# Optimization experiments

Measured on AMD Instinct MI355X. Metric: run time of the kernel, lower is better.

The kernel has to match this reference:

```python
import jax, jax.numpy as jnp
import numpy as np
from jax import lax

B, L, D, H = 48, 512, 384, 384


def setup_inputs() -> dict:
    key = jax.random.key(0)
    ks = jax.random.split(key, 8)
    def w(k, shape, fan):
        return jax.random.normal(k, shape, jnp.float32) / np.float32(np.sqrt(fan))
    return {
        "v": jax.random.normal(ks[0], (B, L, D), jnp.float32),
        "mask": jnp.ones((B, L), jnp.bool_),
        "Wp_cur": w(ks[1], (D, H), D),      # torch Wp (applied to v_i)
        "Wp_seq": w(ks[2], (D, H), D),      # torch Wp_ (applied to all of v)
        "V": w(ks[3], (H,), H),             # torch V: Linear(H, 1, bias=False)
        "W_ih": w(ks[4], (3 * H, 2 * D), 2 * D),  # GRUCell input weights
        "W_hh": w(ks[5], (3 * H, H), H),           # GRUCell hidden weights
        "b_ih": jnp.zeros((3 * H,), jnp.float32),
        "b_hh": jnp.zeros((3 * H,), jnp.float32),
    }


def _forward(v, mask, Wp_cur, Wp_seq, V, W_ih, W_hh, b_ih, b_hh):
    Bv, Lv, _ = v.shape
    Hh = W_hh.shape[1]
    # Torch recomputes Wp_(v) identically every step; hoist it (same math).
    Wpv = jnp.einsum('bld,dh->blh', v, Wp_seq)            # [B,L,H]
    neg = jnp.where(mask, 0.0, -1e30).astype(v.dtype)     # additive attention mask [B,L]

    def step(h, vi):                                       # vi: [B,D], h: [B,H]
        wpi = vi @ Wp_cur                                  # [B,H]
        x = jnp.tanh(Wpv + wpi[:, None, :])                # [B,L,H]
        s = jnp.einsum('blh,h->bl', x, V) + neg            # scores [B,L]
        a = jax.nn.softmax(s, axis=1)                      # masked softmax
        c = jnp.einsum('bl,bld->bd', a, v)                 # context [B,D]
        r = jnp.concatenate([vi, c], axis=1)               # [B,2D]
        gi = r @ W_ih.T + b_ih
        gh = h @ W_hh.T + b_hh
        ir, iz, inn = jnp.split(gi, 3, axis=1)
        hr, hz, hn = jnp.split(gh, 3, axis=1)
        rg = jax.nn.sigmoid(ir + hr)
        zg = jax.nn.sigmoid(iz + hz)
        ng = jnp.tanh(inn + rg * hn)
        hnew = (1.0 - zg) * ng + zg * h                    # PyTorch GRUCell update
        return hnew, hnew

    h0 = jnp.zeros((Bv, Hh), v.dtype)
    h_last, hs = lax.scan(jax.checkpoint(step), h0, jnp.swapaxes(v, 0, 1))
    hs = jnp.swapaxes(hs, 0, 1)                            # [B,L,H]
    # dropout p=0.0 -> identity; h = hs[:, -1]
    return hs, h_last


def reference(v, mask, Wp_cur, Wp_seq, V, W_ih, W_hh, b_ih, b_hh):
    return _forward(v, mask, Wp_cur, Wp_seq, V, W_ih, W_hh, b_ih, b_hh)
```

## Files before the change

### kernel.cpp

```cpp
#include <hip/hip_runtime.h>


typedef unsigned short u16;
typedef unsigned int u32;
typedef short short8 __attribute__((ext_vector_type(8)));
typedef float f32x4 __attribute__((ext_vector_type(4)));
typedef float f4 __attribute__((ext_vector_type(4)));
typedef _Float16 h2_t __attribute__((ext_vector_type(2)));
typedef _Float16 h8_t __attribute__((ext_vector_type(8)));

#define BDIM 48
#define LDIM 512
#define DDIM 384
#define HDIM 384

__device__ __forceinline__ float bf2f(u16 u) { return __uint_as_float(((u32)u) << 16); }
__device__ __forceinline__ u16 f2bf(float f) {
  u32 x = __float_as_uint(f);
  u32 r = (x + 0x7fffu + ((x >> 16) & 1u)) >> 16;
  return (u16)r;
}
__device__ __forceinline__ float sigm(float x) {
  return __builtin_amdgcn_rcpf(1.f + exp2f(-1.4426950408889634f * x));
}
__device__ __forceinline__ float tanh_f(float x) {
  float e = exp2f(2.885390081777927f * x);
  return 1.f - 2.f * __builtin_amdgcn_rcpf(e + 1.f);
}

__device__ __forceinline__ void load16(const void* src, long ld, int isf32,
                                       long row, int kbase, short8& o0, short8& o1)
{
  if (isf32) {
    const float* s = (const float*)src + row * ld + kbase;
    f4 q0 = *(const f4*)(s);
    f4 q1 = *(const f4*)(s + 4);
    f4 q2 = *(const f4*)(s + 8);
    f4 q3 = *(const f4*)(s + 12);
    short8 a, b;
    a[0] = (short)f2bf(q0[0]); a[1] = (short)f2bf(q0[1]);
    a[2] = (short)f2bf(q0[2]); a[3] = (short)f2bf(q0[3]);
    a[4] = (short)f2bf(q1[0]); a[5] = (short)f2bf(q1[1]);
    a[6] = (short)f2bf(q1[2]); a[7] = (short)f2bf(q1[3]);
    b[0] = (short)f2bf(q2[0]); b[1] = (short)f2bf(q2[1]);
    b[2] = (short)f2bf(q2[2]); b[3] = (short)f2bf(q2[3]);
    b[4] = (short)f2bf(q3[0]); b[5] = (short)f2bf(q3[1]);
    b[6] = (short)f2bf(q3[2]); b[7] = (short)f2bf(q3[3]);
    o0 = a; o1 = b;
  } else {
    const u16* s = (const u16*)src + row * ld + kbase;
    o0 = *(const short8*)s;
    o1 = *(const short8*)(s + 8);
  }
}

__global__ __launch_bounds__(256) void gemm_bt(
    const void* __restrict__ A1, const void* __restrict__ A2,
    long lda1, long lda2, int ksplit, int a1f, int a2f,
    const void* __restrict__ Bm, long ldb, int bfm,
    u16* __restrict__ Out, int N, int K,
    long strideA, long strideB, long strideO,
    const float* __restrict__ bias, int epi_exp2, int out_bf16)
{
  __shared__ u16 As[128][40];
  __shared__ u16 Bs[128][40];
  const int tid = threadIdx.x;
  const int lane = tid & 63;
  const int w = tid >> 6;
  const int wm = w >> 1, wn = w & 1;
  const int l15 = lane & 15, quad = lane >> 4;
  const long m0 = (long)blockIdx.x * 128;
  const long n0 = (long)blockIdx.y * 128;
  const int z = blockIdx.z;
  const char* A1p = (const char*)A1 + (long)z * strideA * (a1f ? 4 : 2);
  const char* A2p = (const char*)A2 + (long)z * strideA * (a2f ? 4 : 2);
  const char* Bp  = (const char*)Bm + (long)z * strideB * (bfm ? 4 : 2);
  u16* Op = Out + (long)z * strideO;

  const int r2 = tid & 127;
  const int half = tid >> 7;

  f32x4 acc[4][4];
#pragma unroll
  for (int a = 0; a < 4; a++)
#pragma unroll
    for (int c = 0; c < 4; c++) acc[a][c] = (f32x4){0.f, 0.f, 0.f, 0.f};

  for (int k0 = 0; k0 < K; k0 += 32) {
    const void* srcA; long lda; int kk; int af;
    if (k0 < ksplit) { srcA = A1p; lda = lda1; kk = k0; af = a1f; }
    else             { srcA = A2p; lda = lda2; kk = k0 - ksplit; af = a2f; }
    short8 a0, a1, b0, b1;
    load16(srcA, lda, af, m0 + r2, kk + half * 16, a0, a1);
    load16(Bp, ldb, bfm, n0 + r2, k0 + half * 16, b0, b1);
    __syncthreads();
    *(short8*)&As[r2][half * 16] = a0;
    *(short8*)&As[r2][half * 16 + 8] = a1;
    *(short8*)&Bs[r2][half * 16] = b0;
    *(short8*)&Bs[r2][half * 16 + 8] = b1;
    __syncthreads();
    short8 af_[4], bf_[4];
#pragma unroll
    for (int mt = 0; mt < 4; mt++) af_[mt] = *(const short8*)&As[wm * 64 + mt * 16 + l15][quad * 8];
#pragma unroll
    for (int nt = 0; nt < 4; nt++) bf_[nt] = *(const short8*)&Bs[wn * 64 + nt * 16 + l15][quad * 8];
#pragma unroll
    for (int mt = 0; mt < 4; mt++)
#pragma unroll
      for (int nt = 0; nt < 4; nt++)
        acc[mt][nt] = __builtin_amdgcn_mfma_f32_16x16x32_bf16(af_[mt], bf_[nt], acc[mt][nt], 0, 0, 0);
  }

#pragma unroll
  for (int mt = 0; mt < 4; mt++) {
#pragma unroll
    for (int nt = 0; nt < 4; nt++) {
      const long col = n0 + wn * 64 + nt * 16 + l15;
      float bv = bias ? bias[col] : 0.f;
#pragma unroll
      for (int rg = 0; rg < 4; rg++) {
        long row = m0 + wm * 64 + mt * 16 + quad * 4 + rg;
        float vv = acc[mt][nt][rg] + bv;
        if (epi_exp2) {
          float t = vv * 2.885390081777927f;
          t = fminf(fmaxf(t, -15.9f), 15.9f);
          vv = exp2f(t);
        }
        long idx = row * (long)N + col;
        if (out_bf16) Op[idx] = f2bf(vv);
        else ((_Float16*)Op)[idx] = (_Float16)vv;
      }
    }
  }
}

__global__ void transpose_f2b(const float* __restrict__ src, u16* __restrict__ dst,
                              int rows, int cols, long sstride, long dstride)
{
  __shared__ float t[32][33];
  const int bz = blockIdx.z;
  const float* s = src + (long)bz * sstride;
  u16* d = dst + (long)bz * dstride;
  const int c0 = blockIdx.x * 32, r0 = blockIdx.y * 32;
  const int tx = threadIdx.x, ty = threadIdx.y;
#pragma unroll
  for (int j = 0; j < 4; j++) t[ty + j * 8][tx] = s[(long)(r0 + ty + j * 8) * cols + c0 + tx];
  __syncthreads();
#pragma unroll
  for (int j = 0; j < 4; j++) d[(long)(c0 + ty + j * 8) * rows + r0 + tx] = f2bf(t[tx][ty + j * 8]);
}

__global__ __launch_bounds__(256) void attn_softmax(
    const _Float16* __restrict__ E, const _Float16* __restrict__ F,
    const float* __restrict__ Vw, u16* __restrict__ Aout)
{
  const int blk = blockIdx.x;
  const int x8 = blk & 7;
  const int rest = blk >> 3;
  const int i = rest & 511;
  const int b = x8 + 8 * (rest >> 9);
  const int tid = threadIdx.x;
  const int lane = tid & 63, w = tid >> 6;
  const int r = lane & 15, sub = lane >> 4;
  __shared__ float Tl[512];
  __shared__ float red[8];

  const h8_t* Fr = (const h8_t*)(F + ((long)b * LDIM + i) * HDIM + r * 24);
  h8_t fq0 = Fr[0], fq1 = Fr[1], fq2 = Fr[2];
  float fv[24], vv[24];
#pragma unroll
  for (int j = 0; j < 8; j++) {
    fv[j] = (float)fq0[j]; fv[8 + j] = (float)fq1[j]; fv[16 + j] = (float)fq2[j];
  }
  const float* Vp = Vw + r * 24;
#pragma unroll
  for (int j = 0; j < 24; j++) vv[j] = Vp[j];

  for (int li = 0; li < 32; ++li) {
    const int l = li * 16 + w * 4 + sub;
    const h8_t* Er = (const h8_t*)(E + ((long)b * LDIM + l) * HDIM + r * 24);
    h8_t e0 = Er[0], e1 = Er[1], e2 = Er[2];
    float p = 0.f;
#pragma unroll
    for (int j = 0; j < 8; j++) {
      p += vv[j]      * __builtin_amdgcn_rcpf((float)e0[j] * fv[j]      + 1.f);
      p += vv[8 + j]  * __builtin_amdgcn_rcpf((float)e1[j] * fv[8 + j]  + 1.f);
      p += vv[16 + j] * __builtin_amdgcn_rcpf((float)e2[j] * fv[16 + j] + 1.f);
    }
    p += __shfl_xor(p, 1);
    p += __shfl_xor(p, 2);
    p += __shfl_xor(p, 4);
    p += __shfl_xor(p, 8);
    if (r == 0) Tl[l] = p;
  }
  __syncthreads();

  const float t0 = Tl[tid], t1 = Tl[tid + 256];
  float mn = fminf(t0, t1);
#pragma unroll
  for (int off = 32; off; off >>= 1) mn = fminf(mn, __shfl_xor(mn, off));
  if (lane == 0) red[w] = mn;
  __syncthreads();
  const float mT = fminf(fminf(red[0], red[1]), fminf(red[2], red[3]));
  const float C2 = 2.885390081777927f;
  float p0 = exp2f(C2 * (mT - t0));
  float p1 = exp2f(C2 * (mT - t1));
  float ssum = p0 + p1;
#pragma unroll
  for (int off = 32; off; off >>= 1) ssum += __shfl_xor(ssum, off);
  if (lane == 0) red[4 + w] = ssum;
  __syncthreads();
  const float Z = (red[4] + red[5]) + (red[6] + red[7]);
  const float inv = __builtin_amdgcn_rcpf(Z);
  u16* Ar = Aout + ((long)b * LDIM + i) * LDIM;
  Ar[tid] = f2bf(p0 * inv);
  Ar[tid + 256] = f2bf(p1 * inv);
}

__global__ __launch_bounds__(512, 2) void recurrence(
    const float* __restrict__ Whh, const float* __restrict__ bhh_g,
    const _Float16* __restrict__ GI, u32* __restrict__ hslots,
    float* __restrict__ out)
{
  const int blk = blockIdx.x;
  const int x8 = blk & 7;
  const int s = blk >> 3;
  const int b = x8 + 8 * (s % 6);
  const int g = s / 6;
  const int tid = threadIdx.x;
  const int tx = tid & 15;
  const int ty = tid >> 4;

  __shared__ _Float16 hall[HDIM];
  __shared__ float gh[288];

  h2_t wv[9][12];
  float bh[9];
#pragma unroll
  for (int q = 0; q < 9; q++) {
    int rr = ty * 9 + q;
    int R = (rr / 96) * 384 + g * 96 + (rr % 96);
    const f4* wq = (const f4*)(Whh + (long)R * HDIM + tx * 24);
#pragma unroll
    for (int t6 = 0; t6 < 6; t6++) {
      f4 u = wq[t6];
      wv[q][2 * t6]     = (h2_t){(_Float16)u[0], (_Float16)u[1]};
      wv[q][2 * t6 + 1] = (h2_t){(_Float16)u[2], (_Float16)u[3]};
    }
    bh[q] = (tx == 0) ? bhh_g[R] : 0.f;
  }

  if (tid < HDIM) hall[tid] = (_Float16)0.f;
  __syncthreads();

  const long gi_base = (long)b * LDIM * 1152;
  const int own = tid >> 5;
  (void)own;
  float hprev = 0.f;

  for (int i = 0; i < LDIM; ++i) {
    float gir = 0.f, giz = 0.f, gin = 0.f;
    if (tid < 96) {
      const long gb = gi_base + (long)i * 1152 + g * 96 + tid;
      gir = (float)GI[gb];
      giz = (float)GI[gb + 384];
      gin = (float)GI[gb + 768];
    }

    if (i > 0) {
      if (tid < HDIM && (tid / 96) != g) {
        u32* p = hslots + (long)(i & 1) * (BDIM * HDIM) + (long)b * HDIM + tid;
        u32 val = __hip_atomic_load(p, __ATOMIC_RELAXED, __HIP_MEMORY_SCOPE_AGENT);
        while ((val >> 16) != (u32)i) {
          __builtin_amdgcn_s_sleep(1);
          val = __hip_atomic_load(p, __ATOMIC_RELAXED, __HIP_MEMORY_SCOPE_AGENT);
        }
        union { u16 u; _Float16 h; } cv;
        cv.u = (u16)val;
        hall[tid] = cv.h;
      }
      __syncthreads();
    }

    h2_t hv[12];
#pragma unroll
    for (int p = 0; p < 12; p++) hv[p] = *(const h2_t*)&hall[tx * 24 + 2 * p];
    float ac[9];
#pragma unroll
    for (int q = 0; q < 9; q++) {
      float a = 0.f;
#pragma unroll
      for (int p = 0; p < 12; p++) a = __builtin_amdgcn_fdot2(wv[q][p], hv[p], a, false);
      ac[q] = a;
    }
#pragma unroll
    for (int q = 0; q < 9; q++) {
      float a = ac[q];
      a += __shfl_xor(a, 1);
      a += __shfl_xor(a, 2);
      a += __shfl_xor(a, 4);
      a += __shfl_xor(a, 8);
      if (tx == 0) gh[ty * 9 + q] = a + bh[q];
    }
    __syncthreads();
    if (tid < 96) {
      const int j = g * 96 + tid;
      float hr = gh[tid], hz = gh[96 + tid], hn = gh[192 + tid];
      float rg = sigm(gir + hr);
      float zg = sigm(giz + hz);
      float ng = tanh_f(gin + rg * hn);
      float hnew = (1.f - zg) * ng + zg * hprev;
      hprev = hnew;
      out[((long)b * LDIM + i) * HDIM + j] = hnew;
      if (i == LDIM - 1) out[(long)BDIM * LDIM * HDIM + (long)b * HDIM + j] = hnew;
      union { _Float16 h; u16 u; } cv;
      cv.h = (_Float16)hnew;
      hall[j] = cv.h;
      if (i + 1 < LDIM) {
        u32 val = ((u32)(i + 1) << 16) | (u32)cv.u;
        __hip_atomic_store(
            hslots + (long)((i + 1) & 1) * (BDIM * HDIM) + (long)b * HDIM + j, val,
            __ATOMIC_RELAXED, __HIP_MEMORY_SCOPE_AGENT);
      }
    }
  }
}

extern "C" void kernel_launch(void* const* d_in, const int* in_sizes, int n_in,
                              void* d_out, int out_size, void* d_ws, size_t ws_size,
                              hipStream_t stream)
{
  (void)in_sizes; (void)n_in; (void)out_size; (void)ws_size;
  const float* v      = (const float*)d_in[0];
  const float* Wp_cur = (const float*)d_in[2];
  const float* Wp_seq = (const float*)d_in[3];
  const float* Vw     = (const float*)d_in[4];
  const float* W_ih   = (const float*)d_in[5];
  const float* W_hh   = (const float*)d_in[6];
  const float* b_ih   = (const float*)d_in[7];
  const float* b_hh   = (const float*)d_in[8];
  float* out = (float*)d_out;

  char* ws = (char*)d_ws;
  size_t off = 0;
  auto alloc = [&](size_t bytes) -> char* {
    char* p = ws + off;
    off += (bytes + 255) & ~(size_t)255;
    return p;
  };
  u32* hslots = (u32*)alloc((size_t)2 * 48 * 384 * 4);
  u16* WpSeqT = (u16*)alloc((size_t)384 * 384 * 2);
  u16* WpCurT = (u16*)alloc((size_t)384 * 384 * 2);
  u16* Cbuf   = (u16*)alloc((size_t)24576 * 384 * 2);
  u16* vT     = (u16*)alloc((size_t)48 * 384 * 512 * 2);
  char* region = alloc((size_t)24576 * 384 * 2 * 2 + (size_t)24576 * 512 * 2);
  _Float16* E  = (_Float16*)region;
  _Float16* F  = (_Float16*)(region + (size_t)24576 * 384 * 2);
  u16* Abuf    = (u16*)(region + (size_t)24576 * 384 * 2 * 2);
  _Float16* GI = (_Float16*)region;

  transpose_f2b<<<dim3(12, 12, 1), dim3(32, 8), 0, stream>>>(Wp_seq, WpSeqT, 384, 384, 0, 0);
  transpose_f2b<<<dim3(12, 12, 1), dim3(32, 8), 0, stream>>>(Wp_cur, WpCurT, 384, 384, 0, 0);
  transpose_f2b<<<dim3(12, 16, 48), dim3(32, 8), 0, stream>>>(v, vT, 512, 384,
                                                              (long)512 * 384, (long)384 * 512);

  gemm_bt<<<dim3(192, 3, 1), 256, 0, stream>>>(v, v, 384, 384, 1 << 30, 1, 1,
                                               WpSeqT, 384, 0,
                                               (u16*)E, 384, 384, 0, 0, 0, nullptr, 1, 0);
  gemm_bt<<<dim3(192, 3, 1), 256, 0, stream>>>(v, v, 384, 384, 1 << 30, 1, 1,
                                               WpCurT, 384, 0,
                                               (u16*)F, 384, 384, 0, 0, 0, nullptr, 1, 0);

  attn_softmax<<<dim3(24576), 256, 0, stream>>>(E, F, Vw, Abuf);

  gemm_bt<<<dim3(4, 3, 48), 256, 0, stream>>>(Abuf, Abuf, 512, 512, 1 << 30, 0, 0,
                                              vT, 512, 0,
                                              Cbuf, 384, 512,
                                              (long)512 * 512, (long)384 * 512, (long)512 * 384,
                                              nullptr, 0, 1);

  gemm_bt<<<dim3(192, 9, 1), 256, 0, stream>>>(v, Cbuf, 384, 384, 384, 1, 0,
                                               W_ih, 768, 1,
                                               (u16*)GI, 1152, 768, 0, 0, 0, b_ih, 0, 0);

  void* args[] = {(void*)&W_hh, (void*)&b_hh, (void*)&GI, (void*)&hslots, (void*)&out};
  hipLaunchCooperativeKernel(recurrence, dim3(192), dim3(512), args, 0, stream);
}
```

Baseline: 2.342 ms.

## Tile four query rows per attention block and prefetch GI in recurrence

```diff
diff --git a/kernel.cpp b/kernel.cpp
--- a/kernel.cpp
+++ b/kernel.cpp
@@ -19,6 +19,9 @@
   u32 x = __float_as_uint(f);
   u32 r = (x + 0x7fffu + ((x >> 16) & 1u)) >> 16;
   return (u16)r;
+}
+__device__ __forceinline__ float h16f(u16 u) {
+  union { u16 u; _Float16 h; } c; c.u = u; return (float)c.h;
 }
 __device__ __forceinline__ float sigm(float x) {
   return __builtin_amdgcn_rcpf(1.f + exp2f(-1.4426950408889634f * x));
@@ -157,20 +160,23 @@
   const int blk = blockIdx.x;
   const int x8 = blk & 7;
   const int rest = blk >> 3;
-  const int i = rest & 511;
-  const int b = x8 + 8 * (rest >> 9);
+  const int ig = rest & 127;
+  const int b = x8 + 8 * (rest >> 7);
+  const int i0 = ig * 4;
   const int tid = threadIdx.x;
   const int lane = tid & 63, w = tid >> 6;
   const int r = lane & 15, sub = lane >> 4;
-  __shared__ float Tl[512];
-  __shared__ float red[8];
-
-  const h8_t* Fr = (const h8_t*)(F + ((long)b * LDIM + i) * HDIM + r * 24);
-  h8_t fq0 = Fr[0], fq1 = Fr[1], fq2 = Fr[2];
-  float fv[24], vv[24];
-#pragma unroll
-  for (int j = 0; j < 8; j++) {
-    fv[j] = (float)fq0[j]; fv[8 + j] = (float)fq1[j]; fv[16 + j] = (float)fq2[j];
+  __shared__ float Tl[4][512];
+
+  float fv[4][24], vv[24];
+#pragma unroll
+  for (int ii = 0; ii < 4; ii++) {
+    const h8_t* Fr = (const h8_t*)(F + ((long)b * LDIM + i0 + ii) * HDIM + r * 24);
+    h8_t q0 = Fr[0], q1 = Fr[1], q2 = Fr[2];
+#pragma unroll
+    for (int j = 0; j < 8; j++) {
+      fv[ii][j] = (float)q0[j]; fv[ii][8 + j] = (float)q1[j]; fv[ii][16 + j] = (float)q2[j];
+    }
   }
   const float* Vp = Vw + r * 24;
 #pragma unroll
@@ -180,46 +186,51 @@
     const int l = li * 16 + w * 4 + sub;
     const h8_t* Er = (const h8_t*)(E + ((long)b * LDIM + l) * HDIM + r * 24);
     h8_t e0 = Er[0], e1 = Er[1], e2 = Er[2];
-    float p = 0.f;
+    float ev[24];
 #pragma unroll
     for (int j = 0; j < 8; j++) {
-      p += vv[j]      * __builtin_amdgcn_rcpf((float)e0[j] * fv[j]      + 1.f);
-      p += vv[8 + j]  * __builtin_amdgcn_rcpf((float)e1[j] * fv[8 + j]  + 1.f);
-      p += vv[16 + j] * __builtin_amdgcn_rcpf((float)e2[j] * fv[16 + j] + 1.f);
-    }
-    p += __shfl_xor(p, 1);
-    p += __shfl_xor(p, 2);
-    p += __shfl_xor(p, 4);
-    p += __shfl_xor(p, 8);
-    if (r == 0) Tl[l] = p;
+      ev[j] = (float)e0[j]; ev[8 + j] = (float)e1[j]; ev[16 + j] = (float)e2[j];
+    }
+    float p[4] = {0.f, 0.f, 0.f, 0.f};
+#pragma unroll
+    for (int j = 0; j < 24; j++) {
+#pragma unroll
+      for (int ii = 0; ii < 4; ii++)
+        p[ii] += vv[j] * __builtin_amdgcn_rcpf(ev[j] * fv[ii][j] + 1.f);
+    }
+#pragma unroll
+    for (int ii = 0; ii < 4; ii++) {
+      float q = p[ii];
+      q += __shfl_xor(q, 1);
+      q += __shfl_xor(q, 2);
+      q += __shfl_xor(q, 4);
+      q += __shfl_xor(q, 8);
+      if (r == 0) Tl[ii][l] = q;
+    }
   }
   __syncthreads();
 
-  const float t0 = Tl[tid], t1 = Tl[tid + 256];
-  float mn = fminf(t0, t1);
+  float t[8];
+  float mn = 1e30f;
+#pragma unroll
+  for (int k = 0; k < 8; k++) { t[k] = Tl[w][lane + 64 * k]; mn = fminf(mn, t[k]); }
 #pragma unroll
   for (int off = 32; off; off >>= 1) mn = fminf(mn, __shfl_xor(mn, off));
-  if (lane == 0) red[w] = mn;
-  __syncthreads();
-  const float mT = fminf(fminf(red[0], red[1]), fminf(red[2], red[3]));
   const float C2 = 2.885390081777927f;
-  float p0 = exp2f(C2 * (mT - t0));
-  float p1 = exp2f(C2 * (mT - t1));
-  float ssum = p0 + p1;
-#pragma unroll
-  for (int off = 32; off; off >>= 1) ssum += __shfl_xor(ssum, off);
-  if (lane == 0) red[4 + w] = ssum;
-  __syncthreads();
-  const float Z = (red[4] + red[5]) + (red[6] + red[7]);
+  float p8[8], Z = 0.f;
+#pragma unroll
+  for (int k = 0; k < 8; k++) { p8[k] = exp2f(C2 * (mn - t[k])); Z += p8[k]; }
+#pragma unroll
+  for (int off = 32; off; off >>= 1) Z += __shfl_xor(Z, off);
   const float inv = __builtin_amdgcn_rcpf(Z);
-  u16* Ar = Aout + ((long)b * LDIM + i) * LDIM;
-  Ar[tid] = f2bf(p0 * inv);
-  Ar[tid + 256] = f2bf(p1 * inv);
+  u16* Ar = Aout + ((long)b * LDIM + i0 + w) * LDIM;
+#pragma unroll
+  for (int k = 0; k < 8; k++) Ar[lane + 64 * k] = f2bf(p8[k] * inv);
 }
 
 __global__ __launch_bounds__(512, 2) void recurrence(
     const float* __restrict__ Whh, const float* __restrict__ bhh_g,
-    const _Float16* __restrict__ GI, u32* __restrict__ hslots,
+    const u16* __restrict__ GIu, u32* __restrict__ hslots,
     float* __restrict__ out)
 {
   const int blk = blockIdx.x;
@@ -254,32 +265,31 @@
   __syncthreads();
 
   const long gi_base = (long)b * LDIM * 1152;
-  const int own = tid >> 5;
-  (void)own;
   float hprev = 0.f;
+  u16 c0 = 0, c1 = 0, c2 = 0;
+  if (tid < 96) {
+    const long gb = gi_base + g * 96 + tid;
+    c0 = GIu[gb]; c1 = GIu[gb + 384]; c2 = GIu[gb + 768];
+  }
 
   for (int i = 0; i < LDIM; ++i) {
-    float gir = 0.f, giz = 0.f, gin = 0.f;
-    if (tid < 96) {
-      const long gb = gi_base + (long)i * 1152 + g * 96 + tid;
-      gir = (float)GI[gb];
-      giz = (float)GI[gb + 384];
-      gin = (float)GI[gb + 768];
-    }
-
     if (i > 0) {
       if (tid < HDIM && (tid / 96) != g) {
         u32* p = hslots + (long)(i & 1) * (BDIM * HDIM) + (long)b * HDIM + tid;
         u32 val = __hip_atomic_load(p, __ATOMIC_RELAXED, __HIP_MEMORY_SCOPE_AGENT);
-        while ((val >> 16) != (u32)i) {
-          __builtin_amdgcn_s_sleep(1);
+        while ((val >> 16) != (u32)i)
           val = __hip_atomic_load(p, __ATOMIC_RELAXED, __HIP_MEMORY_SCOPE_AGENT);
-        }
         union { u16 u; _Float16 h; } cv;
         cv.u = (u16)val;
         hall[tid] = cv.h;
       }
       __syncthreads();
+    }
+
+    u16 n0 = 0, n1 = 0, n2 = 0;
+    if (tid < 96 && i + 1 < LDIM) {
+      const long gb = gi_base + (long)(i + 1) * 1152 + g * 96 + tid;
+      n0 = GIu[gb]; n1 = GIu[gb + 384]; n2 = GIu[gb + 768];
     }
 
     h2_t hv[12];
@@ -306,23 +316,24 @@
     if (tid < 96) {
       const int j = g * 96 + tid;
       float hr = gh[tid], hz = gh[96 + tid], hn = gh[192 + tid];
-      float rg = sigm(gir + hr);
-      float zg = sigm(giz + hz);
-      float ng = tanh_f(gin + rg * hn);
+      float rg = sigm(h16f(c0) + hr);
+      float zg = sigm(h16f(c1) + hz);
+      float ng = tanh_f(h16f(c2) + rg * hn);
       float hnew = (1.f - zg) * ng + zg * hprev;
       hprev = hnew;
-      out[((long)b * LDIM + i) * HDIM + j] = hnew;
-      if (i == LDIM - 1) out[(long)BDIM * LDIM * HDIM + (long)b * HDIM + j] = hnew;
       union { _Float16 h; u16 u; } cv;
       cv.h = (_Float16)hnew;
-      hall[j] = cv.h;
       if (i + 1 < LDIM) {
         u32 val = ((u32)(i + 1) << 16) | (u32)cv.u;
         __hip_atomic_store(
             hslots + (long)((i + 1) & 1) * (BDIM * HDIM) + (long)b * HDIM + j, val,
             __ATOMIC_RELAXED, __HIP_MEMORY_SCOPE_AGENT);
       }
-    }
+      hall[j] = cv.h;
+      out[((long)b * LDIM + i) * HDIM + j] = hnew;
+      if (i == LDIM - 1) out[(long)BDIM * LDIM * HDIM + (long)b * HDIM + j] = hnew;
+    }
+    c0 = n0; c1 = n1; c2 = n2;
   }
 }
 
@@ -371,7 +382,7 @@
                                                WpCurT, 384, 0,
                                                (u16*)F, 384, 384, 0, 0, 0, nullptr, 1, 0);
 
-  attn_softmax<<<dim3(24576), 256, 0, stream>>>(E, F, Vw, Abuf);
+  attn_softmax<<<dim3(6144), 256, 0, stream>>>(E, F, Vw, Abuf);
 
   gemm_bt<<<dim3(4, 3, 48), 256, 0, stream>>>(Abuf, Abuf, 512, 512, 1 << 30, 0, 0,
                                               vT, 512, 0,
```

Result: no change. 2.344 ms (+0.0%).
